# Optimization experiments

Hardware: AMD Instinct MI355X
Metric: run time of the kernel (lower is better)

The kernel has to match this reference:

```python
import jax, jax.numpy as jnp
import numpy as np

B, T, D, V, L = 128, 1024, 512, 128, 128
BLANK = V - 1          # keras ctc_batch_cost uses num_classes-1 as blank
EPS = 1e-7             # tf.keras.backend.epsilon()
NEG = jnp.float32(-1e30)


def setup_inputs() -> dict:
    key = jax.random.key(0)
    k1, k2, k3, k4 = jax.random.split(key, 4)
    x = jax.random.normal(k1, (B, T, D), jnp.float32)
    W = jax.random.normal(k2, (D, V), jnp.float32) / np.sqrt(D)
    b = jnp.zeros((V,), jnp.float32)
    targets = jax.random.randint(k3, (B, L), 0, V - 1, dtype=jnp.int32)   # labels in [0, V-2]
    targets_length = jax.random.randint(k4, (B,), 16, L + 1, dtype=jnp.int32)  # >=1
    return {"x": x, "W": W, "b": b, "targets": targets, "targets_length": targets_length}


def _ctc_neg_log_lik(log_probs, targets, targets_length):
    # log_probs: [B,T,V]; targets: [B,L]; returns per-example -log p(targets | probs)
    Bb, Tt, Vv = log_probs.shape
    Ll = targets.shape[1]
    S = 2 * Ll + 1
    # extended label sequence: blank, l1, blank, l2, ..., blank   [B,S]
    ext = jnp.full((Bb, S), BLANK, dtype=targets.dtype)
    ext = ext.at[:, 1::2].set(targets)
    # allow skip transition s-2 -> s when ext[s] != blank and ext[s] != ext[s-2]
    ext2 = jnp.concatenate([jnp.full((Bb, 2), -1, ext.dtype), ext[:, :-2]], axis=1)
    allow2 = (ext != BLANK) & (ext != ext2)                       # [B,S]

    def emit(logp_t):  # logp_t [B,V] -> [B,S]
        return jnp.take_along_axis(logp_t, ext, axis=1)

    # t = 0: only s=0 (blank) and s=1 (first label) reachable
    e0 = emit(log_probs[:, 0])
    alpha0 = jnp.where(jnp.arange(S)[None, :] < 2, e0, NEG)       # [B,S]

    def step(alpha, logp_t):
        a1 = jnp.concatenate([jnp.full((Bb, 1), NEG), alpha[:, :-1]], axis=1)
        a2 = jnp.concatenate([jnp.full((Bb, 2), NEG), alpha[:, :-2]], axis=1)
        m = jnp.logaddexp(alpha, a1)
        m = jnp.where(allow2, jnp.logaddexp(m, a2), m)
        return m + emit(logp_t), None

    alpha_T, _ = jax.lax.scan(step, alpha0, jnp.swapaxes(log_probs, 0, 1)[1:])
    # final states: s = 2*len (trailing blank) and s = 2*len - 1 (last label)
    last = 2 * targets_length                                     # [B]
    aN = jnp.take_along_axis(alpha_T, last[:, None], axis=1)[:, 0]
    aN1 = jnp.take_along_axis(alpha_T, (last - 1)[:, None], axis=1)[:, 0]
    return -jnp.logaddexp(aN, aN1)                                # [B]


def reference(x, W, b, targets, targets_length):
    # Dense -> Softmax (module outputs probabilities) -> ctc_batch_cost: log(p + eps) -> CTC DP -> sum
    probs = jax.nn.softmax(jnp.einsum("btd,dv->btv", x, W) + b, axis=-1)
    log_probs = jnp.log(probs + EPS)
    loss = _ctc_neg_log_lik(log_probs, targets, targets_length)
    return jnp.sum(loss)
```

## Files before the change

### kernel.cpp

```cpp
#include <hip/hip_runtime.h>

#define Bb 128
#define Tt 1024
#define Dd 512
#define Vv 128
#define Ll 128
#define EPSF 1e-7f
#define PADK 72
#define CH 16
#define NEGF -1e30f

typedef float f4 __attribute__((ext_vector_type(4)));
typedef short s8 __attribute__((ext_vector_type(8)));
typedef float f32x4 __attribute__((ext_vector_type(4)));

__device__ inline unsigned int f2bf(float f) {
    unsigned int u = __float_as_uint(f);
    return (u + 0x7fffu + ((u >> 16) & 1u)) >> 16;
}

__device__ inline float lae2(float x, float y) {
    float m = fmaxf(x, y);
    float d = fminf(x, y) - m;
    return m + __logf(1.f + __expf(d));
}

__device__ inline float dpp_shr1(float v) {
    return __int_as_float(__builtin_amdgcn_update_dpp(
        0, __float_as_int(v), 0x138, 0xf, 0xf, false));
}
__device__ inline int dpp_shr1_i(int v) {
    return __builtin_amdgcn_update_dpp(0, v, 0x138, 0xf, 0xf, false);
}

__global__ void wt_kernel(const float* __restrict__ W, unsigned short* __restrict__ Wt) {
    int idx = blockIdx.x * 256 + threadIdx.x;
    int v = idx >> 9, k = idx & 511;
    Wt[idx] = (unsigned short)f2bf(W[k * Vv + v]);
}

__global__ __launch_bounds__(256) void gemm_softmax(
    const float* __restrict__ x, const unsigned short* __restrict__ Wt,
    const float* __restrict__ bias, float* __restrict__ LP)
{
    __shared__ float lds[128 * 128];
    unsigned short* Al = (unsigned short*)lds;
    unsigned short* Bl = Al + 128 * PADK;

    const int tid = threadIdx.x;
    const int wave = tid >> 6, lane = tid & 63;
    const int lm = lane & 15, lq = lane >> 4;
    const int wm = (wave >> 1) << 6, wn = (wave & 1) << 6;
    const long row0 = (long)blockIdx.x << 7;

    f32x4 acc[4][4];
    #pragma unroll
    for (int i = 0; i < 4; i++)
        #pragma unroll
        for (int j = 0; j < 4; j++)
            acc[i][j] = (f32x4){0.f, 0.f, 0.f, 0.f};

    for (int k0 = 0; k0 < Dd; k0 += 64) {
        __syncthreads();
        #pragma unroll
        for (int i = 0; i < 8; i++) {
            int idx = tid + (i << 8);
            int r = idx >> 4, c4 = idx & 15;
            f4 v = *(const f4*)(x + (row0 + r) * Dd + k0 + (c4 << 2));
            unsigned long long q =
                (unsigned long long)(f2bf(v.x) | (f2bf(v.y) << 16)) |
                ((unsigned long long)(f2bf(v.z) | (f2bf(v.w) << 16)) << 32);
            *(unsigned long long*)(Al + r * PADK + (c4 << 2)) = q;
        }
        #pragma unroll
        for (int i = 0; i < 4; i++) {
            int idx = tid + (i << 8);
            int vr = idx >> 3, c = idx & 7;
            f4 w = *(const f4*)(Wt + vr * 512 + k0 + (c << 3));
            *(f4*)(Bl + vr * PADK + (c << 3)) = w;
        }
        __syncthreads();
        #pragma unroll
        for (int kk = 0; kk < 64; kk += 32) {
            s8 af[4], bfr[4];
            #pragma unroll
            for (int mi = 0; mi < 4; mi++)
                af[mi] = *(const s8*)(Al + (wm + (mi << 4) + lm) * PADK + kk + (lq << 3));
            #pragma unroll
            for (int ni = 0; ni < 4; ni++)
                bfr[ni] = *(const s8*)(Bl + (wn + (ni << 4) + lm) * PADK + kk + (lq << 3));
            #pragma unroll
            for (int mi = 0; mi < 4; mi++)
                #pragma unroll
                for (int ni = 0; ni < 4; ni++)
                    acc[mi][ni] = __builtin_amdgcn_mfma_f32_16x16x32_bf16(
                        af[mi], bfr[ni], acc[mi][ni], 0, 0, 0);
        }
    }
    __syncthreads();
    #pragma unroll
    for (int mi = 0; mi < 4; mi++) {
        #pragma unroll
        for (int ni = 0; ni < 4; ni++) {
            int col = wn + (ni << 4) + lm;
            float bv = bias[col];
            #pragma unroll
            for (int r = 0; r < 4; r++) {
                int row = wm + (mi << 4) + (lq << 2) + r;
                int word = (row << 7) + ((((col >> 2) + row) & 31) << 2) + (col & 3);
                lds[word] = acc[mi][ni][r] + bv;
            }
        }
    }
    __syncthreads();
    if (tid < 128) {
        int row = tid;
        float m = -1e30f;
        #pragma unroll
        for (int c = 0; c < 32; c++) {
            int word = (row << 7) + (((c + row) & 31) << 2);
            f4 v = *(const f4*)(lds + word);
            m = fmaxf(m, fmaxf(fmaxf(v.x, v.y), fmaxf(v.z, v.w)));
        }
        float s = 0.f;
        #pragma unroll
        for (int c = 0; c < 32; c++) {
            int word = (row << 7) + (((c + row) & 31) << 2);
            f4 v = *(f4*)(lds + word);
            v.x = __expf(v.x - m); v.y = __expf(v.y - m);
            v.z = __expf(v.z - m); v.w = __expf(v.w - m);
            s += v.x + v.y + v.z + v.w;
            *(f4*)(lds + word) = v;
        }
        float inv = 1.f / s;
        f4* Pout = (f4*)(LP + (row0 + row) * Vv);
        #pragma unroll
        for (int c = 0; c < 32; c++) {
            int word = (row << 7) + (((c + row) & 31) << 2);
            f4 v = *(const f4*)(lds + word);
            v.x = fmaf(v.x, inv, EPSF);
            v.y = fmaf(v.y, inv, EPSF);
            v.z = fmaf(v.z, inv, EPSF);
            v.w = fmaf(v.w, inv, EPSF);
            Pout[c] = v;
        }
    }
}

__global__ __launch_bounds__(64) void ctc_kernel(
    const float* __restrict__ P, const int* __restrict__ targets,
    const int* __restrict__ tlen, float* __restrict__ out)
{
    const int b = blockIdx.x;
    const int lane = threadIdx.x;
    const float* Pb = P + (long)b * Tt * Vv;

    const int tgt0 = targets[(b << 7) + (lane << 1)];
    const int tgt1 = targets[(b << 7) + (lane << 1) + 1];
    int tp = __shfl_up(tgt1, 1);
    if (lane == 0) tp = -1;
    const bool mA = (tgt0 != tp);
    const bool mB = (tgt1 != tgt0);

    const float* pB = Pb + 127;
    const float* p0 = Pb + tgt0;
    const float* p1 = Pb + tgt1;

    float u0 = (lane == 0) ? pB[0] : 0.f;
    float u1 = (lane == 0) ? p0[0] : 0.f;
    float u2 = 0.f, u3 = 0.f, u4 = 0.f;
    int anc = 0;
    float fprev = 1.f;

    float cb[CH], c0[CH], c1[CH];
    #pragma unroll
    for (int i = 0; i < CH; i++) {
        cb[i] = pB[(1 + i) * Vv];
        c0[i] = p0[(1 + i) * Vv];
        c1[i] = p1[(1 + i) * Vv];
    }

    for (int tb = 1; tb < Tt; tb += CH) {
        float nb[CH], q0[CH], q1[CH];
        #pragma unroll
        for (int i = 0; i < CH; i++) {
            int tn = tb + CH + i; if (tn > Tt - 1) tn = Tt - 1;
            nb[i] = pB[tn * Vv]; q0[i] = p0[tn * Vv]; q1[i] = p1[tn * Vv];
        }
        #pragma unroll
        for (int i = 0; i < CH; i++) {
            if (tb + i < Tt) {
                float lb = cb[i], l0 = c0[i], l1 = c1[i];
                float us = dpp_shr1(u3) * fprev;
                float n0 = (u0 + us) * lb;
                float n1 = (u0 + u1 + (mA ? us : 0.f)) * l0;
                float n2 = (u1 + u2) * lb;
                float n3 = (u2 + u3 + (mB ? u1 : 0.f)) * l1;
                float n4 = (u3 + u4) * lb;
                u0 = n0; u1 = n1; u2 = n2; u3 = n3; u4 = n4;
            }
            if ((i & 3) == 3) {
                float umax = fmaxf(fmaxf(fmaxf(u0, u1), fmaxf(u2, u3)), u4);
                bool live = umax > 0.f;
                int e = (int)((__float_as_uint(umax) >> 23) & 0xffu) - 126;
                float sc = __uint_as_float((unsigned)(127 - e) << 23);
                u0 *= sc; u1 *= sc; u2 *= sc; u3 *= sc; u4 *= sc;
                anc = live ? (anc + e) : anc;
                #pragma unroll
                for (int r = 0; r < 3; r++) {
                    int cp_ = dpp_shr1_i(anc);
                    anc = live ? anc : cp_;
                }
                int cp = dpp_shr1_i(anc);
                int d = cp - anc;
                d = d > 96 ? 96 : d;
                fprev = (d < -126) ? 0.f
                       : __uint_as_float((unsigned)((d + 127) << 23));
            }
        }
        #pragma unroll
        for (int i = 0; i < CH; i++) { cb[i] = nb[i]; c0[i] = q0[i]; c1[i] = q1[i]; }
    }

    __shared__ float af[257];
    const float LN2 = 0.69314718056f;
    float fa = (float)anc;
    af[(lane << 2) + 0] = u0 > 0.f ? (fa + log2f(u0)) * LN2 : NEGF;
    af[(lane << 2) + 1] = u1 > 0.f ? (fa + log2f(u1)) * LN2 : NEGF;
    af[(lane << 2) + 2] = u2 > 0.f ? (fa + log2f(u2)) * LN2 : NEGF;
    af[(lane << 2) + 3] = u3 > 0.f ? (fa + log2f(u3)) * LN2 : NEGF;
    if (lane == 63) af[256] = u4 > 0.f ? (fa + log2f(u4)) * LN2 : NEGF;
    __syncthreads();
    if (lane == 0) {
        int len = tlen[b];
        float loss = -lae2(af[2 * len], af[2 * len - 1]);
        atomicAdd(out, loss);
    }
}

extern "C" void kernel_launch(void* const* d_in, const int* in_sizes, int n_in,
                              void* d_out, int out_size, void* d_ws, size_t ws_size,
                              hipStream_t stream) {
    const float* x       = (const float*)d_in[0];
    const float* W       = (const float*)d_in[1];
    const float* bias    = (const float*)d_in[2];
    const int*   targets = (const int*)d_in[3];
    const int*   tl      = (const int*)d_in[4];
    float* out = (float*)d_out;

    float* LP = (float*)d_ws;
    unsigned short* Wt = (unsigned short*)((char*)d_ws + (size_t)Bb * Tt * Vv * 4);

    (void)hipMemsetAsync(out, 0, sizeof(float), stream);
    wt_kernel<<<256, 256, 0, stream>>>(W, Wt);
    gemm_softmax<<<1024, 256, 0, stream>>>(x, Wt, bias, LP);
    ctc_kernel<<<Bb, 64, 0, stream>>>(LP, targets, tl, out);
}
```

Measured before the change: 459.9 us.

## Store probabilities transposed [B,V,T] so CTC reads contiguous time vectors

The GEMM+softmax epilogue now writes probabilities in a [B,V,T] layout, reading each row's scale from shared memory and emitting float4 stores along time. The CTC kernel then loads 16 consecutive timesteps per class as four float4 vector loads instead of 16 scalar loads strided by V. The goal is to turn the latency-bound strided gathers in the serial CTC recurrence into fewer, wider loads. The trade-off is a more scattered, bank-conflict-prone LDS read pattern in the epilogue, plus an extra sync.

```diff
diff --git a/kernel.cpp b/kernel.cpp
--- a/kernel.cpp
+++ b/kernel.cpp
@@ -7,7 +7,6 @@
 #define Ll 128
 #define EPSF 1e-7f
 #define PADK 72
-#define CH 16
 #define NEGF -1e30f
 
 typedef float f4 __attribute__((ext_vector_type(4)));
@@ -44,6 +43,7 @@
     const float* __restrict__ bias, float* __restrict__ LP)
 {
     __shared__ float lds[128 * 128];
+    __shared__ float invs[128];
     unsigned short* Al = (unsigned short*)lds;
     unsigned short* Bl = Al + 128 * PADK;
 
@@ -132,28 +132,36 @@
             s += v.x + v.y + v.z + v.w;
             *(f4*)(lds + word) = v;
         }
-        float inv = 1.f / s;
-        f4* Pout = (f4*)(LP + (row0 + row) * Vv);
-        #pragma unroll
-        for (int c = 0; c < 32; c++) {
-            int word = (row << 7) + (((c + row) & 31) << 2);
-            f4 v = *(const f4*)(lds + word);
-            v.x = fmaf(v.x, inv, EPSF);
-            v.y = fmaf(v.y, inv, EPSF);
-            v.z = fmaf(v.z, inv, EPSF);
-            v.w = fmaf(v.w, inv, EPSF);
-            Pout[c] = v;
+        invs[row] = 1.f / s;
+    }
+    __syncthreads();
+    {
+        const int v = tid >> 1, h = tid & 1;
+        const int bidx = blockIdx.x >> 3;
+        const int tbase = (blockIdx.x & 7) << 7;
+        float* dst = LP + ((long)bidx * Vv + v) * Tt + tbase + (h << 6);
+        const int c0w = v >> 2, r0 = v & 3;
+        #pragma unroll
+        for (int j4 = 0; j4 < 16; j4++) {
+            f4 o;
+            #pragma unroll
+            for (int jj = 0; jj < 4; jj++) {
+                int t = (h << 6) + (j4 << 2) + jj;
+                int word = (t << 7) + (((c0w + t) & 31) << 2) + r0;
+                o[jj] = fmaf(lds[word], invs[t], EPSF);
+            }
+            *(f4*)(dst + (j4 << 2)) = o;
         }
     }
 }
 
 __global__ __launch_bounds__(64) void ctc_kernel(
-    const float* __restrict__ P, const int* __restrict__ targets,
+    const float* __restrict__ PT, const int* __restrict__ targets,
     const int* __restrict__ tlen, float* __restrict__ out)
 {
     const int b = blockIdx.x;
     const int lane = threadIdx.x;
-    const float* Pb = P + (long)b * Tt * Vv;
+    const float* baseP = PT + (long)b * Vv * Tt;
 
     const int tgt0 = targets[(b << 7) + (lane << 1)];
     const int tgt1 = targets[(b << 7) + (lane << 1) + 1];
@@ -162,9 +170,9 @@
     const bool mA = (tgt0 != tp);
     const bool mB = (tgt1 != tgt0);
 
-    const float* pB = Pb + 127;
-    const float* p0 = Pb + tgt0;
-    const float* p1 = Pb + tgt1;
+    const float* pB = baseP + 127 * Tt;
+    const float* p0 = baseP + (long)tgt0 * Tt;
+    const float* p1 = baseP + (long)tgt1 * Tt;
 
     float u0 = (lane == 0) ? pB[0] : 0.f;
     float u1 = (lane == 0) ? p0[0] : 0.f;
@@ -172,25 +180,28 @@
     int anc = 0;
     float fprev = 1.f;
 
-    float cb[CH], c0[CH], c1[CH];
+    f4 cb[4], c0[4], c1[4];
     #pragma unroll
-    for (int i = 0; i < CH; i++) {
-        cb[i] = pB[(1 + i) * Vv];
-        c0[i] = p0[(1 + i) * Vv];
-        c1[i] = p1[(1 + i) * Vv];
-    }
-
-    for (int tb = 1; tb < Tt; tb += CH) {
-        float nb[CH], q0[CH], q1[CH];
-        #pragma unroll
-        for (int i = 0; i < CH; i++) {
-            int tn = tb + CH + i; if (tn > Tt - 1) tn = Tt - 1;
-            nb[i] = pB[tn * Vv]; q0[i] = p0[tn * Vv]; q1[i] = p1[tn * Vv];
-        }
-        #pragma unroll
-        for (int i = 0; i < CH; i++) {
-            if (tb + i < Tt) {
-                float lb = cb[i], l0 = c0[i], l1 = c1[i];
+    for (int q = 0; q < 4; q++) {
+        cb[q] = *(const f4*)(pB + (q << 2));
+        c0[q] = *(const f4*)(p0 + (q << 2));
+        c1[q] = *(const f4*)(p1 + (q << 2));
+    }
+
+    for (int w = 0; w < 64; w++) {
+        f4 nb[4], q0[4], q1[4];
+        const int tn = (w < 63) ? ((w + 1) << 4) : 1008;
+        #pragma unroll
+        for (int q = 0; q < 4; q++) {
+            nb[q] = *(const f4*)(pB + tn + (q << 2));
+            q0[q] = *(const f4*)(p0 + tn + (q << 2));
+            q1[q] = *(const f4*)(p1 + tn + (q << 2));
+        }
+        const int tb = w << 4;
+        #pragma unroll
+        for (int i = 0; i < 16; i++) {
+            if (tb + i > 0) {
+                float lb = cb[i >> 2][i & 3], l0 = c0[i >> 2][i & 3], l1 = c1[i >> 2][i & 3];
                 float us = dpp_shr1(u3) * fprev;
                 float n0 = (u0 + us) * lb;
                 float n1 = (u0 + u1 + (mA ? us : 0.f)) * l0;
@@ -219,7 +230,7 @@
             }
         }
         #pragma unroll
-        for (int i = 0; i < CH; i++) { cb[i] = nb[i]; c0[i] = q0[i]; c1[i] = q1[i]; }
+        for (int q = 0; q < 4; q++) { cb[q] = nb[q]; c0[q] = q0[q]; c1[q] = q1[q]; }
     }
 
     __shared__ float af[257];
```

New measurement: 447.7 us. 2.7% less time.
